# Kernel optimization log

Hardware: AMD Instinct MI355X
Metric: run time of the kernel (lower is better)

Reference implementation:

```python
import jax, jax.numpy as jnp
import numpy as np

N_NODES = 50000
N_EDGES = 500000
D_IN = 128
D_OUT = 128
BN_EPS = 1e-5


def setup_inputs() -> dict:
    key = jax.random.key(0)
    k0, k1, k2, k3, k4 = jax.random.split(key, 5)
    edge_attr = jax.random.normal(k0, (N_EDGES, D_IN), jnp.float32)
    node_attr = jax.random.normal(k1, (N_NODES, D_IN), jnp.float32)
    row = jax.random.randint(k2, (N_EDGES,), 0, N_NODES)  # senders
    col = jax.random.randint(k3, (N_EDGES,), 0, N_NODES)  # receivers
    W = jax.random.normal(k4, (D_OUT, 3 * D_IN), jnp.float32) / jnp.sqrt(3.0 * D_IN)
    b = jnp.zeros((D_OUT,), jnp.float32)
    gamma = jnp.ones((D_OUT,), jnp.float32)
    beta = jnp.zeros((D_OUT,), jnp.float32)
    return {"edge_attr": edge_attr, "node_attr": node_attr, "W": W, "b": b,
            "gamma": gamma, "beta": beta, "row": row, "col": col}


def reference(edge_attr, node_attr, W, b, gamma, beta, row, col):
    # scatter-sum edge features to receiver and sender nodes  [N_NODES, D_IN]
    recv = jax.ops.segment_sum(edge_attr, col, num_segments=N_NODES)
    send = jax.ops.segment_sum(edge_attr, row, num_segments=N_NODES)
    # concat(receivers_aggr, senders_aggr, node_attr)  [N_NODES, 3*D_IN]
    x = jnp.concatenate([recv, send, node_attr], axis=-1)
    # Linear projection + ReLU (dropout p=0.0 -> identity)
    h = jax.nn.relu(x @ W.T + b)
    # BatchNorm1d (training-mode batch stats, biased variance)
    mu = jnp.mean(h, axis=0)
    var = jnp.mean((h - mu) ** 2, axis=0)
    return gamma * (h - mu) * jax.lax.rsqrt(var + BN_EPS) + beta
```

## Files before the change

kernel.cpp:

```cpp
#include <hip/hip_runtime.h>
#include <hip/hip_bf16.h>

#define N_NODES 50000
#define N_EDGES 500000
#define D_IN    128
#define D_K     384
#define D_OUT   128
#define BN_EPS  1e-5f
#define N_TASK  (2 * N_NODES)
#define NB_SCAN ((N_TASK + 1023) / 1024)
#define NBX     ((N_NODES + 127) / 128)
#define PSTRIDE 400

typedef __bf16 bf16x8 __attribute__((ext_vector_type(8)));
typedef __bf16 bf16x4 __attribute__((ext_vector_type(4)));
typedef float  f32x4  __attribute__((ext_vector_type(4)));

#define OFF_AGG   0ULL
#define OFF_CNT   25600000ULL
#define OFF_OFF   26000000ULL
#define OFF_EID   26400256ULL
#define OFF_RKC   30400256ULL
#define OFF_RKR   32400256ULL
#define OFF_WBF   34400256ULL
#define OFF_PSTAT 34498560ULL
#define OFF_SCALE 34908160ULL
#define OFF_SHIFT 34908672ULL
#define OFF_BSUM  34909184ULL
#define OFF_BOFF  34909696ULL

__global__ void wcvt_kernel(const float* __restrict__ W, __bf16* __restrict__ Wb) {
    int i = blockIdx.x * blockDim.x + threadIdx.x;
    if (i < D_OUT * D_K) Wb[i] = (__bf16)W[i];
}

__global__ __launch_bounds__(256) void hist_kernel(const int* __restrict__ row,
                                                   const int* __restrict__ col,
                                                   int* __restrict__ cnt,
                                                   int* __restrict__ rank_c,
                                                   int* __restrict__ rank_r) {
    int i = blockIdx.x * blockDim.x + threadIdx.x;
    if (i < N_EDGES) {
        rank_c[i] = atomicAdd(&cnt[col[i]], 1);
        rank_r[i] = atomicAdd(&cnt[N_NODES + row[i]], 1);
    }
}

__global__ __launch_bounds__(1024) void partial_kernel(const int* __restrict__ cnt,
                                                       int* __restrict__ bsum) {
    __shared__ int s[1024];
    const int idx = blockIdx.x * 1024 + threadIdx.x;
    s[threadIdx.x] = (idx < N_TASK) ? cnt[idx] : 0;
    __syncthreads();
    for (int ofs = 512; ofs > 0; ofs >>= 1) {
        if (threadIdx.x < ofs) s[threadIdx.x] += s[threadIdx.x + ofs];
        __syncthreads();
    }
    if (threadIdx.x == 0) bsum[blockIdx.x] = s[0];
}

__global__ void bscan_kernel(const int* __restrict__ bsum, int* __restrict__ boff) {
    if (threadIdx.x == 0) {
        int run = 0;
        for (int i = 0; i < NB_SCAN; ++i) { boff[i] = run; run += bsum[i]; }
        boff[NB_SCAN] = run;
    }
}

__global__ __launch_bounds__(1024) void scanfin_kernel(const int* __restrict__ cnt,
                                                       const int* __restrict__ boff,
                                                       int* __restrict__ off) {
    __shared__ int s[1024];
    const int idx = blockIdx.x * 1024 + threadIdx.x;
    const int v = (idx < N_TASK) ? cnt[idx] : 0;
    s[threadIdx.x] = v;
    __syncthreads();
    for (int ofs = 1; ofs < 1024; ofs <<= 1) {
        int t = (threadIdx.x >= ofs) ? s[threadIdx.x - ofs] : 0;
        __syncthreads();
        s[threadIdx.x] += t;
        __syncthreads();
    }
    const int excl = boff[blockIdx.x] + s[threadIdx.x] - v;
    if (idx < N_TASK) off[idx] = excl;
    if (idx == N_TASK - 1) off[N_TASK] = excl + v;
}

__global__ __launch_bounds__(256) void sid_kernel(const int* __restrict__ row,
                                                  const int* __restrict__ col,
                                                  const int* __restrict__ off,
                                                  const int* __restrict__ rank_c,
                                                  const int* __restrict__ rank_r,
                                                  int* __restrict__ eid) {
    int i = blockIdx.x * blockDim.x + threadIdx.x;
    if (i < N_EDGES) {
        eid[off[col[i]] + rank_c[i]] = i;
        eid[off[N_NODES + row[i]] + rank_r[i]] = i;
    }
}

__global__ __launch_bounds__(256) void gather_kernel(const float* __restrict__ edge_attr,
                                                     const int* __restrict__ off,
                                                     const int* __restrict__ eid,
                                                     __bf16* __restrict__ agg) {
    const int lane = threadIdx.x & 63;
    const int wid  = blockIdx.x * 4 + (threadIdx.x >> 6);
    if (wid >= N_TASK) return;
    const int beg = off[wid];
    const int end = off[wid + 1];
    const int hh  = lane >> 5;
    const int c   = (lane & 31) * 4;
    f32x4 acc0 = (f32x4)0.0f, acc1 = (f32x4)0.0f;

    for (int cbeg = beg; cbeg < end; cbeg += 16) {
        const int n = min(16, end - cbeg);
        const int e_reg = (lane < n) ? eid[cbeg + lane] : 0;
#pragma unroll
        for (int k = 0; k < 8; ++k) {
            const int jj = 2 * k + hh;
            const int e  = __shfl(e_reg, jj);
            if (jj < n) {
                const f32x4 v = *(const f32x4*)(edge_attr + (size_t)e * D_IN + c);
                if (k & 1) acc1 += v; else acc0 += v;
            }
        }
    }
    acc0 += acc1;

#pragma unroll
    for (int q = 0; q < 4; ++q) acc0[q] += __shfl_xor(acc0[q], 32);

    if (lane < 32) {
        bf16x4 o;
#pragma unroll
        for (int q = 0; q < 4; ++q) o[q] = (__bf16)acc0[q];
        *(bf16x4*)(agg + (size_t)wid * D_IN + c) = o;
    }
}

#define ROW_B 768
__global__ __launch_bounds__(256) void gemm_kernel(
    const __bf16* __restrict__ agg, const float* __restrict__ node_attr,
    const __bf16* __restrict__ Wb, const float* __restrict__ bias,
    float* __restrict__ h, float* __restrict__ pstat) {
    __shared__ __align__(16) char Ws[64 * ROW_B];
    __shared__ float sred[2][4][64];

    const int lane = threadIdx.x & 63;
    const int w    = threadIdx.x >> 6;
    const int m    = lane & 15;
    const int g    = lane >> 4;
    const int cy   = blockIdx.y;

    {
        const __bf16* src = Wb + (size_t)cy * 64 * D_K;
#pragma unroll
        for (int i = 0; i < 12; ++i) {
            const int idx = i * 256 + threadIdx.x;
            const int r   = idx / 48;
            const int cb  = (idx % 48) * 16;
            bf16x8 v = *(const bf16x8*)(src + (size_t)r * D_K + (idx % 48) * 8);
            *(bf16x8*)(Ws + r * ROW_B + (cb ^ ((r & 7) << 4))) = v;
        }
    }
    __syncthreads();

    const int nodeA0 = blockIdx.x * 128 + w * 32 + m;
    const int nodeA1 = nodeA0 + 16;

    f32x4 acc[2][4];
#pragma unroll
    for (int i = 0; i < 2; ++i)
#pragma unroll
        for (int f = 0; f < 4; ++f) acc[i][f] = (f32x4)0.0f;

#pragma unroll
    for (int ks = 0; ks < 12; ++ks) {
        const int k0 = ks * 32;
        bf16x8 a0, a1;
#pragma unroll
        for (int i = 0; i < 8; ++i) { a0[i] = (__bf16)0.0f; a1[i] = (__bf16)0.0f; }
        if (ks < 8) {
            const size_t base = (size_t)(k0 >> 7) * (N_NODES * D_IN) + (k0 & 127) + g * 8;
            if (nodeA0 < N_NODES) a0 = *(const bf16x8*)(agg + base + (size_t)nodeA0 * D_IN);
            if (nodeA1 < N_NODES) a1 = *(const bf16x8*)(agg + base + (size_t)nodeA1 * D_IN);
        } else {
            const size_t base = (k0 - 256) + g * 8;
            if (nodeA0 < N_NODES) {
                const float* p = node_attr + (size_t)nodeA0 * D_IN + base;
                f32x4 v0 = *(const f32x4*)p, v1 = *(const f32x4*)(p + 4);
#pragma unroll
                for (int i = 0; i < 4; ++i) { a0[i] = (__bf16)v0[i]; a0[i + 4] = (__bf16)v1[i]; }
            }
            if (nodeA1 < N_NODES) {
                const float* p = node_attr + (size_t)nodeA1 * D_IN + base;
                f32x4 v0 = *(const f32x4*)p, v1 = *(const f32x4*)(p + 4);
#pragma unroll
                for (int i = 0; i < 4; ++i) { a1[i] = (__bf16)v0[i]; a1[i + 4] = (__bf16)v1[i]; }
            }
        }
#pragma unroll
        for (int f = 0; f < 4; ++f) {
            const int r = f * 16 + m;
            const int cb = (k0 + g * 8) * 2;
            bf16x8 bfrag = *(const bf16x8*)(Ws + r * ROW_B + (cb ^ ((r & 7) << 4)));
            acc[0][f] = __builtin_amdgcn_mfma_f32_16x16x32_bf16(a0, bfrag, acc[0][f], 0, 0, 0);
            acc[1][f] = __builtin_amdgcn_mfma_f32_16x16x32_bf16(a1, bfrag, acc[1][f], 0, 0, 0);
        }
    }

#pragma unroll
    for (int f = 0; f < 4; ++f) {
        const int j  = cy * 64 + f * 16 + m;
        const float bj = bias[j];
        float s1 = 0.0f, s2 = 0.0f;
#pragma unroll
        for (int i = 0; i < 2; ++i) {
#pragma unroll
            for (int r = 0; r < 4; ++r) {
                const int nodeC = blockIdx.x * 128 + w * 32 + i * 16 + g * 4 + r;
                float v = acc[i][f][r] + bj;
                v = v > 0.0f ? v : 0.0f;
                if (nodeC < N_NODES) {
                    h[(size_t)nodeC * D_OUT + j] = v;
                    s1 += v;
                    s2 += v * v;
                }
            }
        }
        s1 += __shfl_xor(s1, 16, 64);  s2 += __shfl_xor(s2, 16, 64);
        s1 += __shfl_xor(s1, 32, 64);  s2 += __shfl_xor(s2, 32, 64);
        if (lane < 16) { sred[0][w][f * 16 + m] = s1; sred[1][w][f * 16 + m] = s2; }
    }
    __syncthreads();
    if (threadIdx.x < 128) {
        const int s = threadIdx.x >> 6;
        const int c = threadIdx.x & 63;
        const float v = sred[s][0][c] + sred[s][1][c] + sred[s][2][c] + sred[s][3][c];
        pstat[(size_t)(s * 128 + cy * 64 + c) * PSTRIDE + blockIdx.x] = v;
    }
}

__global__ __launch_bounds__(256) void bn_finalize_kernel(
    const float* __restrict__ pstat, const float* __restrict__ gamma,
    const float* __restrict__ beta, float* __restrict__ scale, float* __restrict__ shift) {
    const int j = blockIdx.x;
    float a1 = 0.0f, a2 = 0.0f;
    for (int b = threadIdx.x; b < NBX; b += 256) {
        a1 += pstat[(size_t)j * PSTRIDE + b];
        a2 += pstat[(size_t)(128 + j) * PSTRIDE + b];
    }
#pragma unroll
    for (int ofs = 32; ofs >= 1; ofs >>= 1) {
        a1 += __shfl_xor(a1, ofs, 64);
        a2 += __shfl_xor(a2, ofs, 64);
    }
    __shared__ float w1[4], w2[4];
    if ((threadIdx.x & 63) == 0) { w1[threadIdx.x >> 6] = a1; w2[threadIdx.x >> 6] = a2; }
    __syncthreads();
    if (threadIdx.x == 0) {
        const float S1 = w1[0] + w1[1] + w1[2] + w1[3];
        const float S2 = w2[0] + w2[1] + w2[2] + w2[3];
        const float inv_n = 1.0f / (float)N_NODES;
        const float mu  = S1 * inv_n;
        const float var = S2 * inv_n - mu * mu;
        const float sc  = gamma[j] * rsqrtf(var + BN_EPS);
        scale[j] = sc;
        shift[j] = beta[j] - mu * sc;
    }
}

__global__ __launch_bounds__(256) void bn_apply_kernel(
    float* __restrict__ h, const float* __restrict__ scale, const float* __restrict__ shift) {
    size_t i = ((size_t)blockIdx.x * blockDim.x + threadIdx.x) * 8;
    if (i >= (size_t)N_NODES * D_OUT) return;
    const int j0 = (int)(i & 127);
    f32x4 a = *(const f32x4*)(h + i);
    f32x4 b = *(const f32x4*)(h + i + 4);
#pragma unroll
    for (int q = 0; q < 4; ++q) {
        a[q] = a[q] * scale[j0 + q]     + shift[j0 + q];
        b[q] = b[q] * scale[j0 + 4 + q] + shift[j0 + 4 + q];
    }
    *(f32x4*)(h + i)     = a;
    *(f32x4*)(h + i + 4) = b;
}

extern "C" void kernel_launch(void* const* d_in, const int* in_sizes, int n_in,
                              void* d_out, int out_size, void* d_ws, size_t ws_size,
                              hipStream_t stream) {
    const float* edge_attr = (const float*)d_in[0];
    const float* node_attr = (const float*)d_in[1];
    const float* W         = (const float*)d_in[2];
    const float* bias      = (const float*)d_in[3];
    const float* gamma     = (const float*)d_in[4];
    const float* beta      = (const float*)d_in[5];
    const int*   row       = (const int*)d_in[6];
    const int*   col       = (const int*)d_in[7];
    float* out = (float*)d_out;

    char* ws = (char*)d_ws;
    __bf16* agg    = (__bf16*)(ws + OFF_AGG);
    int*    cnt    = (int*)(ws + OFF_CNT);
    int*    off    = (int*)(ws + OFF_OFF);
    int*    eid    = (int*)(ws + OFF_EID);
    int*    rank_c = (int*)(ws + OFF_RKC);
    int*    rank_r = (int*)(ws + OFF_RKR);
    __bf16* Wb     = (__bf16*)(ws + OFF_WBF);
    float*  pstat  = (float*)(ws + OFF_PSTAT);
    float*  scale  = (float*)(ws + OFF_SCALE);
    float*  shift  = (float*)(ws + OFF_SHIFT);
    int*    bsum   = (int*)(ws + OFF_BSUM);
    int*    boff   = (int*)(ws + OFF_BOFF);

    hipMemsetAsync(cnt, 0, N_TASK * sizeof(int), stream);

    wcvt_kernel<<<(D_OUT * D_K + 255) / 256, 256, 0, stream>>>(W, Wb);
    hist_kernel<<<(N_EDGES + 255) / 256, 256, 0, stream>>>(row, col, cnt, rank_c, rank_r);
    partial_kernel<<<NB_SCAN, 1024, 0, stream>>>(cnt, bsum);
    bscan_kernel<<<1, 64, 0, stream>>>(bsum, boff);
    scanfin_kernel<<<NB_SCAN, 1024, 0, stream>>>(cnt, boff, off);
    sid_kernel<<<(N_EDGES + 255) / 256, 256, 0, stream>>>(row, col, off, rank_c, rank_r, eid);
    gather_kernel<<<(N_TASK + 3) / 4, 256, 0, stream>>>(edge_attr, off, eid, agg);
    dim3 ggrid(NBX, 2);
    gemm_kernel<<<ggrid, 256, 0, stream>>>(agg, node_attr, Wb, bias, out, pstat);
    bn_finalize_kernel<<<128, 256, 0, stream>>>(pstat, gamma, beta, scale, shift);
    bn_apply_kernel<<<(N_NODES * D_OUT / 8 + 255) / 256, 256, 0, stream>>>(out, scale, shift);
}
```

Before: 212.2 us.

## Fuse weight conversion into GEMM, fold block-offset scan into scanfin, enlarge GEMM tiles

Removes the separate W-to-bf16 conversion kernel by having each GEMM block convert its fp32 weight slice while loading it into shared memory. Removes the single-thread block-offset scan kernel by having every scanfin block redo a small 128-entry scan of block sums in shared memory. Doubles the GEMM block to 512 threads covering 256 nodes, which halves the number of blocks and the per-block weight staging, and the BN partial-stat stride shrinks to match. Together this cuts two kernel launches and some redundant W staging, at the cost of fewer, larger GEMM blocks and repeated tiny scans.

```diff
diff --git a/kernel.cpp b/kernel.cpp
--- a/kernel.cpp
+++ b/kernel.cpp
@@ -9,8 +9,8 @@
 #define BN_EPS  1e-5f
 #define N_TASK  (2 * N_NODES)
 #define NB_SCAN ((N_TASK + 1023) / 1024)
-#define NBX     ((N_NODES + 127) / 128)
-#define PSTRIDE 400
+#define NBX     ((N_NODES + 255) / 256)
+#define PSTRIDE 200
 
 typedef __bf16 bf16x8 __attribute__((ext_vector_type(8)));
 typedef __bf16 bf16x4 __attribute__((ext_vector_type(4)));
@@ -22,17 +22,10 @@
 #define OFF_EID   26400256ULL
 #define OFF_RKC   30400256ULL
 #define OFF_RKR   32400256ULL
-#define OFF_WBF   34400256ULL
-#define OFF_PSTAT 34498560ULL
-#define OFF_SCALE 34908160ULL
-#define OFF_SHIFT 34908672ULL
-#define OFF_BSUM  34909184ULL
-#define OFF_BOFF  34909696ULL
-
-__global__ void wcvt_kernel(const float* __restrict__ W, __bf16* __restrict__ Wb) {
-    int i = blockIdx.x * blockDim.x + threadIdx.x;
-    if (i < D_OUT * D_K) Wb[i] = (__bf16)W[i];
-}
+#define OFF_PSTAT 34400256ULL
+#define OFF_SCALE 34605056ULL
+#define OFF_SHIFT 34605568ULL
+#define OFF_BSUM  34606080ULL
 
 __global__ __launch_bounds__(256) void hist_kernel(const int* __restrict__ row,
                                                    const int* __restrict__ col,
@@ -59,18 +52,22 @@
     if (threadIdx.x == 0) bsum[blockIdx.x] = s[0];
 }
 
-__global__ void bscan_kernel(const int* __restrict__ bsum, int* __restrict__ boff) {
-    if (threadIdx.x == 0) {
-        int run = 0;
-        for (int i = 0; i < NB_SCAN; ++i) { boff[i] = run; run += bsum[i]; }
-        boff[NB_SCAN] = run;
-    }
-}
-
 __global__ __launch_bounds__(1024) void scanfin_kernel(const int* __restrict__ cnt,
-                                                       const int* __restrict__ boff,
+                                                       const int* __restrict__ bsum,
                                                        int* __restrict__ off) {
+    __shared__ int sb[128];
     __shared__ int s[1024];
+    if (threadIdx.x < 128) sb[threadIdx.x] = (threadIdx.x < NB_SCAN) ? bsum[threadIdx.x] : 0;
+    __syncthreads();
+    for (int ofs = 1; ofs < 128; ofs <<= 1) {
+        int t = 0;
+        if (threadIdx.x < 128 && threadIdx.x >= ofs) t = sb[threadIdx.x - ofs];
+        __syncthreads();
+        if (threadIdx.x < 128) sb[threadIdx.x] += t;
+        __syncthreads();
+    }
+    const int boff = (blockIdx.x == 0) ? 0 : sb[blockIdx.x - 1];
+
     const int idx = blockIdx.x * 1024 + threadIdx.x;
     const int v = (idx < N_TASK) ? cnt[idx] : 0;
     s[threadIdx.x] = v;
@@ -81,7 +78,7 @@
         s[threadIdx.x] += t;
         __syncthreads();
     }
-    const int excl = boff[blockIdx.x] + s[threadIdx.x] - v;
+    const int excl = boff + s[threadIdx.x] - v;
     if (idx < N_TASK) off[idx] = excl;
     if (idx == N_TASK - 1) off[N_TASK] = excl + v;
 }
@@ -139,12 +136,12 @@
 }
 
 #define ROW_B 768
-__global__ __launch_bounds__(256) void gemm_kernel(
+__global__ __launch_bounds__(512) void gemm_kernel(
     const __bf16* __restrict__ agg, const float* __restrict__ node_attr,
-    const __bf16* __restrict__ Wb, const float* __restrict__ bias,
+    const float* __restrict__ W, const float* __restrict__ bias,
     float* __restrict__ h, float* __restrict__ pstat) {
     __shared__ __align__(16) char Ws[64 * ROW_B];
-    __shared__ float sred[2][4][64];
+    __shared__ float sred[2][8][64];
 
     const int lane = threadIdx.x & 63;
     const int w    = threadIdx.x >> 6;
@@ -153,19 +150,23 @@
     const int cy   = blockIdx.y;
 
     {
-        const __bf16* src = Wb + (size_t)cy * 64 * D_K;
-#pragma unroll
-        for (int i = 0; i < 12; ++i) {
-            const int idx = i * 256 + threadIdx.x;
+        const float* src = W + (size_t)cy * 64 * D_K;
+#pragma unroll
+        for (int i = 0; i < 6; ++i) {
+            const int idx = i * 512 + threadIdx.x;
             const int r   = idx / 48;
-            const int cb  = (idx % 48) * 16;
-            bf16x8 v = *(const bf16x8*)(src + (size_t)r * D_K + (idx % 48) * 8);
-            *(bf16x8*)(Ws + r * ROW_B + (cb ^ ((r & 7) << 4))) = v;
-        }
-    }
-    __syncthreads();
-
-    const int nodeA0 = blockIdx.x * 128 + w * 32 + m;
+            const int c8  = idx % 48;
+            const float* p = src + (size_t)r * D_K + c8 * 8;
+            f32x4 v0 = *(const f32x4*)p, v1 = *(const f32x4*)(p + 4);
+            bf16x8 v;
+#pragma unroll
+            for (int q = 0; q < 4; ++q) { v[q] = (__bf16)v0[q]; v[q + 4] = (__bf16)v1[q]; }
+            *(bf16x8*)(Ws + r * ROW_B + ((c8 * 16) ^ ((r & 7) << 4))) = v;
+        }
+    }
+    __syncthreads();
+
+    const int nodeA0 = blockIdx.x * 256 + w * 32 + m;
     const int nodeA1 = nodeA0 + 16;
 
     f32x4 acc[2][4];
@@ -218,7 +219,7 @@
         for (int i = 0; i < 2; ++i) {
 #pragma unroll
             for (int r = 0; r < 4; ++r) {
-                const int nodeC = blockIdx.x * 128 + w * 32 + i * 16 + g * 4 + r;
+                const int nodeC = blockIdx.x * 256 + w * 32 + i * 16 + g * 4 + r;
                 float v = acc[i][f][r] + bj;
                 v = v > 0.0f ? v : 0.0f;
                 if (nodeC < N_NODES) {
@@ -236,7 +237,9 @@
     if (threadIdx.x < 128) {
         const int s = threadIdx.x >> 6;
         const int c = threadIdx.x & 63;
-        const float v = sred[s][0][c] + sred[s][1][c] + sred[s][2][c] + sred[s][3][c];
+        float v = 0.0f;
+#pragma unroll
+        for (int q = 0; q < 8; ++q) v += sred[s][q][c];
         pstat[(size_t)(s * 128 + cy * 64 + c) * PSTRIDE + blockIdx.x] = v;
     }
 }
@@ -306,24 +309,20 @@
     int*    eid    = (int*)(ws + OFF_EID);
     int*    rank_c = (int*)(ws + OFF_RKC);
     int*    rank_r = (int*)(ws + OFF_RKR);
-    __bf16* Wb     = (__bf16*)(ws + OFF_WBF);
     float*  pstat  = (float*)(ws + OFF_PSTAT);
     float*  scale  = (float*)(ws + OFF_SCALE);
     float*  shift  = (float*)(ws + OFF_SHIFT);
     int*    bsum   = (int*)(ws + OFF_BSUM);
-    int*    boff   = (int*)(ws + OFF_BOFF);
 
     hipMemsetAsync(cnt, 0, N_TASK * sizeof(int), stream);
 
-    wcvt_kernel<<<(D_OUT * D_K + 255) / 256, 256, 0, stream>>>(W, Wb);
     hist_kernel<<<(N_EDGES + 255) / 256, 256, 0, stream>>>(row, col, cnt, rank_c, rank_r);
     partial_kernel<<<NB_SCAN, 1024, 0, stream>>>(cnt, bsum);
-    bscan_kernel<<<1, 64, 0, stream>>>(bsum, boff);
-    scanfin_kernel<<<NB_SCAN, 1024, 0, stream>>>(cnt, boff, off);
+    scanfin_kernel<<<NB_SCAN, 1024, 0, stream>>>(cnt, bsum, off);
     sid_kernel<<<(N_EDGES + 255) / 256, 256, 0, stream>>>(row, col, off, rank_c, rank_r, eid);
     gather_kernel<<<(N_TASK + 3) / 4, 256, 0, stream>>>(edge_attr, off, eid, agg);
     dim3 ggrid(NBX, 2);
-    gemm_kernel<<<ggrid, 256, 0, stream>>>(agg, node_attr, Wb, bias, out, pstat);
+    gemm_kernel<<<ggrid, 512, 0, stream>>>(agg, node_attr, W, bias, out, pstat);
     bn_finalize_kernel<<<128, 256, 0, stream>>>(pstat, gamma, beta, scale, shift);
     bn_apply_kernel<<<(N_NODES * D_OUT / 8 + 255) / 256, 256, 0, stream>>>(out, scale, shift);
 }
```

After: 201.7 us. 5.0% less time.
